# Kernel optimization log

Hardware: AMD Instinct MI355X
Metric: run time of the kernel (lower is better)

## Reference

```python
import jax, jax.numpy as jnp
import numpy as np
import math

D_MODEL = 2048
NUM_HEADS = 16
D_HEAD = D_MODEL // NUM_HEADS
ROPE_BASE = 10000.0

def _rope(t, pos):
    # t: [b, h, T, d_head]; standard rotate-half RoPE with base 10000.
    T, d = t.shape[-2], t.shape[-1]
    start = max(pos, 0)  # pos < 0 means training / position 0
    inv_freq = 1.0 / (ROPE_BASE ** (jnp.arange(0, d, 2, dtype=jnp.float32) / d))  # [d/2]
    positions = jnp.arange(start, start + T, dtype=jnp.float32)                   # [T]
    ang = positions[:, None] * inv_freq[None, :]                                  # [T, d/2]
    cos, sin = jnp.cos(ang), jnp.sin(ang)
    x1, x2 = t[..., : d // 2], t[..., d // 2 :]
    return jnp.concatenate([x1 * cos - x2 * sin, x1 * sin + x2 * cos], axis=-1)

def setup_inputs() -> dict:
    key = jax.random.key(0)
    kx, kq, kk, kv, kw = jax.random.split(key, 5)
    s = 1.0 / math.sqrt(D_MODEL)
    return {
        "x": jax.random.normal(kx, (2, 2048, D_MODEL), dtype=jnp.float32),
        "q_out": jax.random.normal(kq, (D_MODEL, D_MODEL), dtype=jnp.float32) * s,
        "k_out": jax.random.normal(kk, (D_MODEL, D_MODEL), dtype=jnp.float32) * s,
        "v_out": jax.random.normal(kv, (D_MODEL, D_MODEL), dtype=jnp.float32) * s,
        "w_out": jax.random.normal(kw, (D_MODEL, D_MODEL), dtype=jnp.float32) * s,
        "pos": 0,
    }

def reference(x, q_out, k_out, v_out, w_out, pos):
    b, t, d = x.shape
    h, dh = NUM_HEADS, D_HEAD

    def heads(y):  # [b, t, d] -> [b, h, t, dh]
        return y.reshape(b, t, h, dh).transpose(0, 2, 1, 3)

    q = _rope(heads(jnp.einsum('btd,de->bte', x, q_out)), pos)
    k = _rope(heads(jnp.einsum('btd,de->bte', x, k_out)), pos)
    v = heads(jnp.einsum('btd,de->bte', x, v_out))

    score = jnp.einsum('bhqd,bhkd->bhqk', q, k) / math.sqrt(dh)
    causal = jnp.triu(jnp.ones((t, t), dtype=bool), k=1)  # True above diagonal -> masked
    score = jnp.where(causal, -jnp.inf, score)
    weights = jax.nn.softmax(score, axis=-1)
    ctx = jnp.einsum('bhqk,bhkd->bhqd', weights, v)        # [b, h, t, dh]
    ctx = ctx.transpose(0, 2, 1, 3).reshape(b, t, d)
    return jnp.einsum('btd,de->bte', ctx, w_out)
```

## Files before the change

### kernel.cpp

```cpp
#include <hip/hip_runtime.h>
#include <hip/hip_bf16.h>
#include <math.h>

#define NH 16
#define DH 128
#define DM 2048
#define BB 2
#define TT 2048

typedef unsigned short u16;
typedef __attribute__((ext_vector_type(8))) __bf16 bf16x8;
typedef __attribute__((ext_vector_type(8))) u16 u16x8;
typedef __attribute__((ext_vector_type(4))) u16 u16x4;
typedef __attribute__((ext_vector_type(4))) float f32x4;

__device__ __forceinline__ float bf2f(u16 a){
  union { unsigned u; float f; } v; v.u = ((unsigned)a) << 16; return v.f;
}
__device__ __forceinline__ u16 f2bf(float f){
  union { float f; unsigned u; } v; v.f = f;
  unsigned r = v.u + 0x7fffu + ((v.u >> 16) & 1u);
  return (u16)(r >> 16);
}

typedef const __attribute__((address_space(1))) unsigned int* gas_p;
typedef __attribute__((address_space(3))) unsigned int* las_p;
__device__ __forceinline__ void gl_lds16(const u16* g, u16* lds_uniform_base){
  __builtin_amdgcn_global_load_lds((gas_p)(const void*)g,
                                   (las_p)(void*)lds_uniform_base, 16, 0, 0);
}

__global__ __launch_bounds__(256)
void cvt_f32_bf16(const float* __restrict__ src, u16* __restrict__ dst, int n4){
  const int i = blockIdx.x * 256 + threadIdx.x;
  if (i >= n4) return;
  const f32x4 v = *(const f32x4*)(src + (size_t)i * 4);
  u16x4 o;
  #pragma unroll
  for (int j = 0; j < 4; j++) o[j] = f2bf(v[j]);
  *(u16x4*)(dst + (size_t)i * 4) = o;
}

__global__ __launch_bounds__(256)
void transpose2048(const float* __restrict__ W, u16* __restrict__ Wt){
  __shared__ u16 tile[32][33];
  const int tx = threadIdx.x, ty = threadIdx.y;
  const int bx = blockIdx.x * 32, by = blockIdx.y * 32;
  #pragma unroll
  for (int i = 0; i < 32; i += 8)
    tile[ty + i][tx] = f2bf(W[(size_t)(by + ty + i) * DM + bx + tx]);
  __syncthreads();
  #pragma unroll
  for (int i = 0; i < 32; i += 8)
    Wt[(size_t)(bx + ty + i) * DM + by + tx] = tile[tx][ty + i];
}

__global__ __launch_bounds__(256)
void transpose3(const float* __restrict__ w0, const float* __restrict__ w1,
                const float* __restrict__ w2, u16* __restrict__ dst){
  __shared__ u16 tile[32][33];
  const int z = blockIdx.z;
  const float* W = (z == 0) ? w0 : (z == 1) ? w1 : w2;
  u16* Wt = dst + (size_t)z * DM * DM;
  const int tx = threadIdx.x, ty = threadIdx.y;
  const int bx = blockIdx.x * 32, by = blockIdx.y * 32;
  #pragma unroll
  for (int i = 0; i < 32; i += 8)
    tile[ty + i][tx] = f2bf(W[(size_t)(by + ty + i) * DM + bx + tx]);
  __syncthreads();
  #pragma unroll
  for (int i = 0; i < 32; i += 8)
    Wt[(size_t)(bx + ty + i) * DM + by + tx] = tile[tx][ty + i];
}

__global__ __launch_bounds__(256)
void gemm_bt(const u16* __restrict__ A, const u16* __restrict__ Bt_base,
             void* __restrict__ C0, u16* __restrict__ Ck, u16* __restrict__ Cv,
             int mode0){
  __shared__ u16 As[2][128][32];
  __shared__ u16 Bs[2][128][32];
  const int z = blockIdx.z;
  const u16* Bt = Bt_base + (size_t)z * DM * DM;
  void* C = (z == 0) ? C0 : (z == 1) ? (void*)Ck : (void*)Cv;
  const int mode = (z == 0) ? mode0 : (z == 1) ? 3 : 2;

  const int tid = threadIdx.x;
  const int wave = tid >> 6, lane = tid & 63;
  const int wm = wave & 1, wn = wave >> 1;
  const int row16 = lane & 15, quad = lane >> 4;
  const int m0 = blockIdx.x * 128, n0 = blockIdx.y * 128;

  const f32x4 zero = {0.f, 0.f, 0.f, 0.f};
  f32x4 acc[4][4];
  #pragma unroll
  for (int i = 0; i < 4; i++)
    #pragma unroll
    for (int j = 0; j < 4; j++) acc[i][j] = zero;

  const int srow = lane >> 2;
  const int scol = (lane & 3) * 8;

  for (int k0 = 0; k0 < DM; k0 += 64){
    #pragma unroll
    for (int c = 0; c < 2; c++){
      const int rbase = wave * 32 + c * 16;
      const u16* pa = A  + (size_t)(m0 + rbase + srow) * DM + k0 + scol;
      const u16* pb = Bt + (size_t)(n0 + rbase + srow) * DM + k0 + scol;
      gl_lds16(pa,      &As[0][rbase][0]);
      gl_lds16(pa + 32, &As[1][rbase][0]);
      gl_lds16(pb,      &Bs[0][rbase][0]);
      gl_lds16(pb + 32, &Bs[1][rbase][0]);
    }
    __syncthreads();
    #pragma unroll
    for (int buf = 0; buf < 2; buf++){
      bf16x8 af[4], bfr[4];
      #pragma unroll
      for (int mt = 0; mt < 4; mt++)
        af[mt] = *(const bf16x8*)&As[buf][wm * 64 + mt * 16 + row16][quad * 8];
      #pragma unroll
      for (int nt = 0; nt < 4; nt++)
        bfr[nt] = *(const bf16x8*)&Bs[buf][wn * 64 + nt * 16 + row16][quad * 8];
      #pragma unroll
      for (int mt = 0; mt < 4; mt++)
        #pragma unroll
        for (int nt = 0; nt < 4; nt++)
          acc[mt][nt] = __builtin_amdgcn_mfma_f32_16x16x32_bf16(af[mt], bfr[nt], acc[mt][nt], 0, 0, 0);
    }
    __syncthreads();
  }

  #pragma unroll
  for (int mt = 0; mt < 4; mt++){
    #pragma unroll
    for (int nt = 0; nt < 4; nt++){
      #pragma unroll
      for (int r = 0; r < 4; r++){
        const int m = m0 + wm * 64 + mt * 16 + quad * 4 + r;
        const int n = n0 + wn * 64 + nt * 16 + row16;
        const int b = m >> 11, t = m & (TT - 1);
        const int hh = n >> 7, dh = n & (DH - 1);
        if (mode == 1){
          ((u16*)C)[(((size_t)(b * NH + hh) * TT + t) * DH) + dh] = f2bf(acc[mt][nt][r]);
        } else if (mode == 3){
          const int dhs = dh ^ ((t & 7) << 3);
          ((u16*)C)[(((size_t)(b * NH + hh) * TT + t) * DH) + dhs] = f2bf(acc[mt][nt][r]);
        } else if (mode == 2){
          const int ts = (t & 63) ^ ((dh & 7) << 3);
          ((u16*)C)[(((size_t)(b * NH + hh) * 32 + (t >> 6)) * 8192) + dh * 64 + ts] = f2bf(acc[mt][nt][r]);
        } else {
          ((float*)C)[(size_t)m * DM + n] = acc[mt][nt][r];
        }
      }
    }
  }
}

__global__ __launch_bounds__(256)
void rope2(u16* __restrict__ qb, u16* __restrict__ kb, const int* __restrict__ posp){
  const int idx = blockIdx.x * 256 + threadIdx.x;
  const int pair = idx & 63;
  const int row = idx >> 6;
  const int t = row & (TT - 1);
  int p0 = *posp; if (p0 < 0) p0 = 0;
  const float tf = (float)(p0 + t);
  const size_t base = (size_t)row * DH;
  {
    const float inv = expf(-(float)pair * (9.2103403719761836f / 64.f));
    float sn, cs; sincosf(tf * inv, &sn, &cs);
    const float q1 = bf2f(qb[base + pair]);
    const float q2 = bf2f(qb[base + 64 + pair]);
    qb[base + pair]      = f2bf(q1 * cs - q2 * sn);
    qb[base + 64 + pair] = f2bf(q1 * sn + q2 * cs);
  }
  {
    const int pl = pair ^ ((t & 7) << 3);
    const float inv = expf(-(float)pl * (9.2103403719761836f / 64.f));
    float sn, cs; sincosf(tf * inv, &sn, &cs);
    const float k1 = bf2f(kb[base + pair]);
    const float k2 = bf2f(kb[base + 64 + pair]);
    kb[base + pair]      = f2bf(k1 * cs - k2 * sn);
    kb[base + 64 + pair] = f2bf(k1 * sn + k2 * cs);
  }
}

template<bool MASK>
__device__ __forceinline__ void attn_tile(
    int kt0, int qbase, int wave, int row16, int quad,
    const bf16x8 (&qf)[4],
    u16 (&k_s)[64][128], u16 (&vt_s)[128][64], u16 (&p_s)[4][16][72],
    f32x4 (&o_acc)[8], float (&l_acc)[4])
{
  const float scale = 0.08838834764831845f;
  const f32x4 zero = {0.f, 0.f, 0.f, 0.f};
  const int fx = (row16 & 7) << 3;
  f32x4 s_acc[4];
  #pragma unroll
  for (int nt = 0; nt < 4; nt++) s_acc[nt] = zero;
  #pragma unroll
  for (int st = 0; st < 4; st++)
    #pragma unroll
    for (int nt = 0; nt < 4; nt++){
      const bf16x8 kf = *(const bf16x8*)&k_s[nt * 16 + row16][(st * 32 + quad * 8) ^ fx];
      s_acc[nt] = __builtin_amdgcn_mfma_f32_16x16x32_bf16(qf[st], kf, s_acc[nt], 0, 0, 0);
    }
  #pragma unroll
  for (int r = 0; r < 4; r++){
    float ps = 0.f;
    #pragma unroll
    for (int nt = 0; nt < 4; nt++){
      float p = __expf(s_acc[nt][r] * scale);
      if (MASK){
        const int qr = qbase + quad * 4 + r;
        if (kt0 + nt * 16 + row16 > qr) p = 0.f;
      }
      ps += p;
      p_s[wave][quad * 4 + r][nt * 16 + row16] = f2bf(p);
    }
    l_acc[r] += ps;
  }
  asm volatile("" ::: "memory");

  #pragma unroll
  for (int kk = 0; kk < 2; kk++){
    const bf16x8 pf = *(const bf16x8*)&p_s[wave][row16][kk * 32 + quad * 8];
    #pragma unroll
    for (int nd = 0; nd < 8; nd++){
      const bf16x8 vb = *(const bf16x8*)&vt_s[nd * 16 + row16][(kk * 32 + quad * 8) ^ fx];
      o_acc[nd] = __builtin_amdgcn_mfma_f32_16x16x32_bf16(pf, vb, o_acc[nd], 0, 0, 0);
    }
  }
}

__global__ __launch_bounds__(256)
void attn_fwd(const u16* __restrict__ q, const u16* __restrict__ k,
              const u16* __restrict__ vtg, u16* __restrict__ ctx){
  __shared__ u16 k_s[64][128];
  __shared__ u16 vt_s[128][64];
  __shared__ u16 p_s[4][16][72];
  const int tid = threadIdx.x;
  const int wave = tid >> 6, lane = tid & 63;
  const int row16 = lane & 15, quad = lane >> 4;
  const int bh = blockIdx.y;
  const int q0 = (31 - blockIdx.x) * 64;
  const int qbase = q0 + wave * 16;
  const size_t bho = (size_t)bh * TT * DH;

  bf16x8 qf[4];
  {
    const u16* qp = q + bho + (size_t)(qbase + row16) * DH + quad * 8;
    #pragma unroll
    for (int st = 0; st < 4; st++) qf[st] = *(const bf16x8*)(qp + st * 32);
  }

  float l_acc[4] = {0.f, 0.f, 0.f, 0.f};
  const f32x4 zero = {0.f, 0.f, 0.f, 0.f};
  f32x4 o_acc[8];
  #pragma unroll
  for (int i = 0; i < 8; i++) o_acc[i] = zero;

  const int kl_r = lane >> 4, kl_c = (lane & 15) * 8;
  const int vl_r = lane >> 3, vl_c = (lane & 7) * 8;

  for (int kt0 = 0; kt0 < q0 + 64; kt0 += 64){
    #pragma unroll
    for (int i = 0; i < 4; i++){
      const int rb = wave * 16 + i * 4;
      gl_lds16(k + bho + (size_t)(kt0 + rb + kl_r) * DH + kl_c, &k_s[rb][0]);
    }
    const u16* vpan = vtg + ((size_t)bh * 32 + (kt0 >> 6)) * 8192;
    #pragma unroll
    for (int i = 0; i < 4; i++){
      const int rb = wave * 32 + i * 8;
      gl_lds16(vpan + (size_t)(rb + vl_r) * 64 + vl_c, &vt_s[rb][0]);
    }
    __syncthreads();

    if (kt0 < q0)
      attn_tile<false>(kt0, qbase, wave, row16, quad, qf, k_s, vt_s, p_s, o_acc, l_acc);
    else
      attn_tile<true >(kt0, qbase, wave, row16, quad, qf, k_s, vt_s, p_s, o_acc, l_acc);

    __syncthreads();
  }

  #pragma unroll
  for (int r = 0; r < 4; r++){
    #pragma unroll
    for (int off = 1; off < 16; off <<= 1) l_acc[r] += __shfl_xor(l_acc[r], off, 64);
  }

  const int b = bh >> 4, h = bh & 15;
  #pragma unroll
  for (int nd = 0; nd < 8; nd++){
    #pragma unroll
    for (int r = 0; r < 4; r++){
      const int qr = qbase + quad * 4 + r;
      const size_t off = ((size_t)b * TT + qr) * DM + h * DH + nd * 16 + row16;
      ctx[off] = f2bf(o_acc[nd][r] / l_acc[r]);
    }
  }
}

extern "C" void kernel_launch(void* const* d_in, const int* in_sizes, int n_in,
                              void* d_out, int out_size, void* d_ws, size_t ws_size,
                              hipStream_t stream){
  const float* x  = (const float*)d_in[0];
  const float* wq = (const float*)d_in[1];
  const float* wk = (const float*)d_in[2];
  const float* wv = (const float*)d_in[3];
  const float* wo = (const float*)d_in[4];
  const int* pos  = (const int*)d_in[5];

  char* ws = (char*)d_ws;
  const dim3 tg(64, 64), tb(32, 8);

  if (ws_size >= 92274688ull){
    u16* xb  = (u16*)ws;                  u16* cb = xb;
    u16* wt3 = (u16*)(ws + 16777216);
    u16* qb  = (u16*)(ws + 41943040);
    u16* kb  = (u16*)(ws + 58720256);
    u16* vtg = (u16*)(ws + 75497472);

    cvt_f32_bf16<<<8192, 256, 0, stream>>>(x, xb, 2097152);
    transpose3<<<dim3(64, 64, 3), tb, 0, stream>>>(wq, wk, wv, wt3);
    gemm_bt<<<dim3(32, 16, 3), 256, 0, stream>>>(xb, wt3, qb, kb, vtg, 1);
    transpose2048<<<tg, tb, 0, stream>>>(wo, wt3);
    rope2<<<16384, 256, 0, stream>>>(qb, kb, pos);
    attn_fwd<<<dim3(32, 32), 256, 0, stream>>>(qb, kb, vtg, cb);
    gemm_bt<<<dim3(32, 16, 1), 256, 0, stream>>>(cb, wt3, d_out, 0, 0, 0);
  } else {
    u16* xb  = (u16*)ws;                  u16* cb = xb;
    u16* wt  = (u16*)(ws + 16777216);
    u16* qb  = (u16*)(ws + 25165824);
    u16* kb  = (u16*)(ws + 41943040);
    u16* vtg = (u16*)(ws + 58720256);

    cvt_f32_bf16<<<8192, 256, 0, stream>>>(x, xb, 2097152);
    transpose2048<<<tg, tb, 0, stream>>>(wq, wt);
    gemm_bt<<<dim3(32, 16, 1), 256, 0, stream>>>(xb, wt, qb, 0, 0, 1);
    transpose2048<<<tg, tb, 0, stream>>>(wk, wt);
    gemm_bt<<<dim3(32, 16, 1), 256, 0, stream>>>(xb, wt, kb, 0, 0, 3);
    transpose2048<<<tg, tb, 0, stream>>>(wv, wt);
    gemm_bt<<<dim3(32, 16, 1), 256, 0, stream>>>(xb, wt, vtg, 0, 0, 2);
    rope2<<<16384, 256, 0, stream>>>(qb, kb, pos);
    attn_fwd<<<dim3(32, 32), 256, 0, stream>>>(qb, kb, vtg, cb);
    transpose2048<<<tg, tb, 0, stream>>>(wo, wt);
    gemm_bt<<<dim3(32, 16, 1), 256, 0, stream>>>(cb, wt, d_out, 0, 0, 0);
  }
}
```

Baseline: 458.8 us.

## Double-buffer attention K/V loads, pair causal tiles per block, use fast RoPE trig

The attention kernel now double-buffers the K and V^T shared-memory tiles. The next tile's global-to-LDS loads are issued before computing the current one, with vmcnt waits and raw barriers in place of full __syncthreads. Each block processes two query tiles, (31-i) and i, so every block does the same amount of causal work, and the grid is halved. MFMA sections are wrapped in s_setprio, and RoPE switches to the fast __expf/__sinf/__cosf intrinsics, which are less accurate for large angles. Shared memory per block roughly doubles, which may reduce occupancy.

New measurement: 407.9 us. 11.1% less time.

```diff
diff --git a/kernel.cpp b/kernel.cpp
--- a/kernel.cpp
+++ b/kernel.cpp
@@ -29,6 +29,12 @@
   __builtin_amdgcn_global_load_lds((gas_p)(const void*)g,
                                    (las_p)(void*)lds_uniform_base, 16, 0, 0);
 }
+
+#define SB() do{ asm volatile("" ::: "memory"); \
+                 __builtin_amdgcn_s_barrier();  \
+                 asm volatile("" ::: "memory"); }while(0)
+#define WAITV8 asm volatile("s_waitcnt vmcnt(8)" ::: "memory")
+#define WAITV0 asm volatile("s_waitcnt vmcnt(0)" ::: "memory")
 
 __global__ __launch_bounds__(256)
 void cvt_f32_bf16(const float* __restrict__ src, u16* __restrict__ dst, int n4){
@@ -166,8 +172,9 @@
   const float tf = (float)(p0 + t);
   const size_t base = (size_t)row * DH;
   {
-    const float inv = expf(-(float)pair * (9.2103403719761836f / 64.f));
-    float sn, cs; sincosf(tf * inv, &sn, &cs);
+    const float inv = __expf(-(float)pair * (9.2103403719761836f / 64.f));
+    const float a = tf * inv;
+    const float sn = __sinf(a), cs = __cosf(a);
     const float q1 = bf2f(qb[base + pair]);
     const float q2 = bf2f(qb[base + 64 + pair]);
     qb[base + pair]      = f2bf(q1 * cs - q2 * sn);
@@ -175,8 +182,9 @@
   }
   {
     const int pl = pair ^ ((t & 7) << 3);
-    const float inv = expf(-(float)pl * (9.2103403719761836f / 64.f));
-    float sn, cs; sincosf(tf * inv, &sn, &cs);
+    const float inv = __expf(-(float)pl * (9.2103403719761836f / 64.f));
+    const float a = tf * inv;
+    const float sn = __sinf(a), cs = __cosf(a);
     const float k1 = bf2f(kb[base + pair]);
     const float k2 = bf2f(kb[base + 64 + pair]);
     kb[base + pair]      = f2bf(k1 * cs - k2 * sn);
@@ -197,6 +205,7 @@
   f32x4 s_acc[4];
   #pragma unroll
   for (int nt = 0; nt < 4; nt++) s_acc[nt] = zero;
+  __builtin_amdgcn_s_setprio(1);
   #pragma unroll
   for (int st = 0; st < 4; st++)
     #pragma unroll
@@ -204,6 +213,7 @@
       const bf16x8 kf = *(const bf16x8*)&k_s[nt * 16 + row16][(st * 32 + quad * 8) ^ fx];
       s_acc[nt] = __builtin_amdgcn_mfma_f32_16x16x32_bf16(qf[st], kf, s_acc[nt], 0, 0, 0);
     }
+  __builtin_amdgcn_s_setprio(0);
   #pragma unroll
   for (int r = 0; r < 4; r++){
     float ps = 0.f;
@@ -221,6 +231,7 @@
   }
   asm volatile("" ::: "memory");
 
+  __builtin_amdgcn_s_setprio(1);
   #pragma unroll
   for (int kk = 0; kk < 2; kk++){
     const bf16x8 pf = *(const bf16x8*)&p_s[wave][row16][kk * 32 + quad * 8];
@@ -230,76 +241,100 @@
       o_acc[nd] = __builtin_amdgcn_mfma_f32_16x16x32_bf16(pf, vb, o_acc[nd], 0, 0, 0);
     }
   }
+  __builtin_amdgcn_s_setprio(0);
+}
+
+__device__ __forceinline__ void attn_pass(
+    const u16* __restrict__ q, const u16* __restrict__ k,
+    const u16* __restrict__ vtg, u16* __restrict__ ctx,
+    int q0, int bh, int wave, int lane, int row16, int quad,
+    u16 (&k_s)[2][64][128], u16 (&vt_s)[2][128][64], u16 (&p_s)[4][16][72])
+{
+  const size_t bho = (size_t)bh * TT * DH;
+  const int qbase = q0 + wave * 16;
+  const int nt = (q0 >> 6) + 1;
+
+  bf16x8 qf[4];
+  {
+    const u16* qp = q + bho + (size_t)(qbase + row16) * DH + quad * 8;
+    #pragma unroll
+    for (int st = 0; st < 4; st++) qf[st] = *(const bf16x8*)(qp + st * 32);
+  }
+
+  float l_acc[4] = {0.f, 0.f, 0.f, 0.f};
+  const f32x4 zero = {0.f, 0.f, 0.f, 0.f};
+  f32x4 o_acc[8];
+  #pragma unroll
+  for (int i = 0; i < 8; i++) o_acc[i] = zero;
+
+  const int kl_r = lane >> 4, kl_c = (lane & 15) * 8;
+  const int vl_r = lane >> 3, vl_c = (lane & 7) * 8;
+
+  #define ASTAGE(t, db) do{ \
+    const int kt = (t) * 64; \
+    _Pragma("unroll") \
+    for (int i = 0; i < 4; i++){ \
+      const int rb = wave * 16 + i * 4; \
+      gl_lds16(k + bho + (size_t)(kt + rb + kl_r) * DH + kl_c, &k_s[db][rb][0]); \
+    } \
+    const u16* vpan = vtg + ((size_t)bh * 32 + (t)) * 8192; \
+    _Pragma("unroll") \
+    for (int i = 0; i < 4; i++){ \
+      const int rb = wave * 32 + i * 8; \
+      gl_lds16(vpan + (size_t)(rb + vl_r) * 64 + vl_c, &vt_s[db][rb][0]); \
+    } \
+  }while(0)
+
+  ASTAGE(0, 0);
+  for (int t = 0; t < nt; ++t){
+    const int db = t & 1;
+    if (t + 1 < nt){
+      ASTAGE(t + 1, db ^ 1);
+      WAITV8;
+    } else {
+      WAITV0;
+    }
+    SB();
+    if (t < nt - 1)
+      attn_tile<false>(t * 64, qbase, wave, row16, quad, qf, k_s[db], vt_s[db], p_s, o_acc, l_acc);
+    else
+      attn_tile<true >(t * 64, qbase, wave, row16, quad, qf, k_s[db], vt_s[db], p_s, o_acc, l_acc);
+    SB();
+  }
+  #undef ASTAGE
+
+  #pragma unroll
+  for (int r = 0; r < 4; r++){
+    #pragma unroll
+    for (int off = 1; off < 16; off <<= 1) l_acc[r] += __shfl_xor(l_acc[r], off, 64);
+  }
+
+  const int b = bh >> 4, h = bh & 15;
+  #pragma unroll
+  for (int nd = 0; nd < 8; nd++){
+    #pragma unroll
+    for (int r = 0; r < 4; r++){
+      const int qr = qbase + quad * 4 + r;
+      const size_t off = ((size_t)b * TT + qr) * DM + h * DH + nd * 16 + row16;
+      ctx[off] = f2bf(o_acc[nd][r] / l_acc[r]);
+    }
+  }
 }
 
 __global__ __launch_bounds__(256)
 void attn_fwd(const u16* __restrict__ q, const u16* __restrict__ k,
               const u16* __restrict__ vtg, u16* __restrict__ ctx){
-  __shared__ u16 k_s[64][128];
-  __shared__ u16 vt_s[128][64];
+  __shared__ u16 k_s[2][64][128];
+  __shared__ u16 vt_s[2][128][64];
   __shared__ u16 p_s[4][16][72];
   const int tid = threadIdx.x;
   const int wave = tid >> 6, lane = tid & 63;
   const int row16 = lane & 15, quad = lane >> 4;
+  const int i = blockIdx.x;
   const int bh = blockIdx.y;
-  const int q0 = (31 - blockIdx.x) * 64;
-  const int qbase = q0 + wave * 16;
-  const size_t bho = (size_t)bh * TT * DH;
-
-  bf16x8 qf[4];
-  {
-    const u16* qp = q + bho + (size_t)(qbase + row16) * DH + quad * 8;
-    #pragma unroll
-    for (int st = 0; st < 4; st++) qf[st] = *(const bf16x8*)(qp + st * 32);
-  }
-
-  float l_acc[4] = {0.f, 0.f, 0.f, 0.f};
-  const f32x4 zero = {0.f, 0.f, 0.f, 0.f};
-  f32x4 o_acc[8];
-  #pragma unroll
-  for (int i = 0; i < 8; i++) o_acc[i] = zero;
-
-  const int kl_r = lane >> 4, kl_c = (lane & 15) * 8;
-  const int vl_r = lane >> 3, vl_c = (lane & 7) * 8;
-
-  for (int kt0 = 0; kt0 < q0 + 64; kt0 += 64){
-    #pragma unroll
-    for (int i = 0; i < 4; i++){
-      const int rb = wave * 16 + i * 4;
-      gl_lds16(k + bho + (size_t)(kt0 + rb + kl_r) * DH + kl_c, &k_s[rb][0]);
-    }
-    const u16* vpan = vtg + ((size_t)bh * 32 + (kt0 >> 6)) * 8192;
-    #pragma unroll
-    for (int i = 0; i < 4; i++){
-      const int rb = wave * 32 + i * 8;
-      gl_lds16(vpan + (size_t)(rb + vl_r) * 64 + vl_c, &vt_s[rb][0]);
-    }
-    __syncthreads();
-
-    if (kt0 < q0)
-      attn_tile<false>(kt0, qbase, wave, row16, quad, qf, k_s, vt_s, p_s, o_acc, l_acc);
-    else
-      attn_tile<true >(kt0, qbase, wave, row16, quad, qf, k_s, vt_s, p_s, o_acc, l_acc);
-
-    __syncthreads();
-  }
-
-  #pragma unroll
-  for (int r = 0; r < 4; r++){
-    #pragma unroll
-    for (int off = 1; off < 16; off <<= 1) l_acc[r] += __shfl_xor(l_acc[r], off, 64);
-  }
-
-  const int b = bh >> 4, h = bh & 15;
-  #pragma unroll
-  for (int nd = 0; nd < 8; nd++){
-    #pragma unroll
-    for (int r = 0; r < 4; r++){
-      const int qr = qbase + quad * 4 + r;
-      const size_t off = ((size_t)b * TT + qr) * DM + h * DH + nd * 16 + row16;
-      ctx[off] = f2bf(o_acc[nd][r] / l_acc[r]);
-    }
-  }
+
+  attn_pass(q, k, vtg, ctx, (31 - i) * 64, bh, wave, lane, row16, quad, k_s, vt_s, p_s);
+  attn_pass(q, k, vtg, ctx, i * 64,        bh, wave, lane, row16, quad, k_s, vt_s, p_s);
 }
 
 extern "C" void kernel_launch(void* const* d_in, const int* in_sizes, int n_in,
@@ -327,7 +362,7 @@
     gemm_bt<<<dim3(32, 16, 3), 256, 0, stream>>>(xb, wt3, qb, kb, vtg, 1);
     transpose2048<<<tg, tb, 0, stream>>>(wo, wt3);
     rope2<<<16384, 256, 0, stream>>>(qb, kb, pos);
-    attn_fwd<<<dim3(32, 32), 256, 0, stream>>>(qb, kb, vtg, cb);
+    attn_fwd<<<dim3(16, 32), 256, 0, stream>>>(qb, kb, vtg, cb);
     gemm_bt<<<dim3(32, 16, 1), 256, 0, stream>>>(cb, wt3, d_out, 0, 0, 0);
   } else {
     u16* xb  = (u16*)ws;                  u16* cb = xb;
@@ -344,7 +379,7 @@
     transpose2048<<<tg, tb, 0, stream>>>(wv, wt);
     gemm_bt<<<dim3(32, 16, 1), 256, 0, stream>>>(xb, wt, vtg, 0, 0, 2);
     rope2<<<16384, 256, 0, stream>>>(qb, kb, pos);
-    attn_fwd<<<dim3(32, 32), 256, 0, stream>>>(qb, kb, vtg, cb);
+    attn_fwd<<<dim3(16, 32), 256, 0, stream>>>(qb, kb, vtg, cb);
     transpose2048<<<tg, tb, 0, stream>>>(wo, wt);
     gemm_bt<<<dim3(32, 16, 1), 256, 0, stream>>>(cb, wt, d_out, 0, 0, 0);
   }
```
